# Performance work log

Hardware: AMD Instinct MI355X
Metric: run time of the kernel (lower is better)

## Reference

```python
import jax, jax.numpy as jnp
import numpy as np

N = 200000   # non-empty octree nodes
K = 27       # 3x3x3 neighborhood taps
C = 64       # channels (in == out, stride 1)
EPS = 1e-5


def octree_conv(x, neigh, W):
    # x: [N, Cin], neigh: [N, K] indices into rows of x, W: [K, Cin, Cout]
    g = x[neigh]                      # gather -> [N, K, Cin] (irregular access)
    return jnp.einsum('nkc,kcd->nd', g, W)


def batch_norm(x, gamma, beta):
    # training-mode BatchNorm1d over the node dimension
    mean = jnp.mean(x, axis=0)
    var = jnp.var(x, axis=0)
    return (x - mean) * jax.lax.rsqrt(var + EPS) * gamma + beta


def setup_inputs() -> dict:
    key = jax.random.key(0)
    ks = jax.random.split(key, 4)
    x = jax.random.normal(ks[0], (N, C), dtype=jnp.float32)
    neigh = jax.random.randint(ks[1], (N, K), 0, N, dtype=jnp.int64)
    scale = 1.0 / np.sqrt(K * C)
    W1 = jax.random.normal(ks[2], (K, C, C), dtype=jnp.float32) * scale
    W2 = jax.random.normal(ks[3], (K, C, C), dtype=jnp.float32) * scale
    return {
        'x': x, 'neigh': neigh, 'depth': 5,
        'W1': W1, 'gamma1': jnp.ones((C,), jnp.float32), 'beta1': jnp.zeros((C,), jnp.float32),
        'W2': W2, 'gamma2': jnp.ones((C,), jnp.float32), 'beta2': jnp.zeros((C,), jnp.float32),
    }


def reference(x, neigh, depth, W1, gamma1, beta1, W2, gamma2, beta2):
    residual = x
    out = octree_conv(x, neigh, W1)
    out = jax.nn.relu(batch_norm(out, gamma1, beta1))
    out = octree_conv(out, neigh, W2)   # stride == 1 -> same depth, same neighborhood
    out = batch_norm(out, gamma2, beta2)
    out = jax.nn.relu(out + residual)   # downsample is None for stride 1
    return (out, depth)
```

## Files before the change

### kernel.cpp

```cpp
#include <hip/hip_runtime.h>

typedef __attribute__((ext_vector_type(8))) short bf16x8;
typedef __attribute__((ext_vector_type(4))) float f32x4;

static __device__ __forceinline__ unsigned short f2bf(float f) {
    unsigned int u = __builtin_bit_cast(unsigned int, f);
    u += 0x7fffu + ((u >> 16) & 1u);
    return (unsigned short)(u >> 16);
}
static __device__ __forceinline__ float bf2f(unsigned short h) {
    unsigned int u = ((unsigned int)h) << 16;
    return __builtin_bit_cast(float, u);
}


__global__ void cvt_x_kernel(const float* __restrict__ x, unsigned short* __restrict__ xb, int total8) {
    int i = blockIdx.x * blockDim.x + threadIdx.x;
    if (i >= total8) return;
    const float4* p = reinterpret_cast<const float4*>(x) + (size_t)i * 2;
    float4 a = p[0], b = p[1];
    bf16x8 o;
    o[0] = (short)f2bf(a.x); o[1] = (short)f2bf(a.y); o[2] = (short)f2bf(a.z); o[3] = (short)f2bf(a.w);
    o[4] = (short)f2bf(b.x); o[5] = (short)f2bf(b.y); o[6] = (short)f2bf(b.z); o[7] = (short)f2bf(b.w);
    reinterpret_cast<bf16x8*>(xb)[i] = o;
}

__global__ void cvt_w_kernel(const float* __restrict__ w1, const float* __restrict__ w2,
                             unsigned short* __restrict__ wt1, unsigned short* __restrict__ wt2) {
    int i = blockIdx.x * blockDim.x + threadIdx.x;
    if (i >= 2 * 27 * 4096) return;
    const float* w = (i < 27 * 4096) ? w1 : w2;
    unsigned short* wt = (i < 27 * 4096) ? wt1 : wt2;
    int j = (i < 27 * 4096) ? i : i - 27 * 4096;
    int k = j >> 12;
    int cout = (j >> 6) & 63;
    int cin = j & 63;
    wt[j] = f2bf(w[((size_t)(k * 64 + cin)) * 64 + cout]);
}

__global__ __launch_bounds__(256, 6) void conv_mfma(
    const unsigned short* __restrict__ xb,
    const int* __restrict__ nh,
    const unsigned short* __restrict__ wt,
    unsigned short* __restrict__ y,
    float* __restrict__ pS,
    float* __restrict__ pQ,
    int n)
{
    __shared__ unsigned short Atile[2][4096];
    __shared__ int lidx[27 * 64];

    const int tid  = threadIdx.x;
    const int wid  = tid >> 6;
    const int lane = tid & 63;
    const int lr   = lane & 15;
    const int lg   = lane >> 4;
    const int base = blockIdx.x * 64;

    for (int j = tid; j < 27 * 64; j += 256) {
        int row = j / 27;
        int kk  = j - row * 27;
        int gr  = base + row; if (gr >= n) gr = n - 1;
        lidx[j] = nh[(size_t)gr * 27 + kk];
    }
    __syncthreads();

    const int srow = tid >> 3;
    const int xoff = ((tid & 7) ^ (srow & 7)) * 8;
    const int so0  = srow * 27;
    const int so1  = (srow + 32) * 27;

    f32x4 acc[4];
    #pragma unroll
    for (int t = 0; t < 4; ++t) acc[t] = (f32x4){0.f, 0.f, 0.f, 0.f};

    const unsigned short* wB = wt + (wid * 16 + lr) * 64 + lg * 8;

#define ISSUE_TILE(kk, b) do {                                                        \
        const int i0_ = lidx[so0 + (kk)];                                             \
        const int i1_ = lidx[so1 + (kk)];                                             \
        __builtin_amdgcn_global_load_lds(                                             \
            (const __attribute__((address_space(1))) unsigned int*)(xb + (size_t)i0_ * 64 + xoff), \
            (__attribute__((address_space(3))) unsigned int*)(&Atile[b][wid * 512]), 16, 0, 0);    \
        __builtin_amdgcn_global_load_lds(                                             \
            (const __attribute__((address_space(1))) unsigned int*)(xb + (size_t)i1_ * 64 + xoff), \
            (__attribute__((address_space(3))) unsigned int*)(&Atile[b][2048 + wid * 512]), 16, 0, 0); \
    } while (0)

    auto compute = [&](const unsigned short* At, bf16x8 B0, bf16x8 B1) {
        #pragma unroll
        for (int t = 0; t < 4; ++t) {
            const int row = t * 16 + lr;
            const int sw  = (row & 7) * 8;
            bf16x8 A0 = *reinterpret_cast<const bf16x8*>(&At[row * 64 + ((lg * 8) ^ sw)]);
            bf16x8 A1 = *reinterpret_cast<const bf16x8*>(&At[row * 64 + (((4 + lg) * 8) ^ sw)]);
            acc[t] = __builtin_amdgcn_mfma_f32_16x16x32_bf16(A0, B0, acc[t], 0, 0, 0);
            acc[t] = __builtin_amdgcn_mfma_f32_16x16x32_bf16(A1, B1, acc[t], 0, 0, 0);
        }
    };

    bf16x8 Ba0 = *reinterpret_cast<const bf16x8*>(wB);
    bf16x8 Ba1 = *reinterpret_cast<const bf16x8*>(wB + 32);
    ISSUE_TILE(0, 0);

    for (int k = 0; k < 26; k += 2) {
        bf16x8 Bb0 = *reinterpret_cast<const bf16x8*>(wB + (k + 1) * 4096);
        bf16x8 Bb1 = *reinterpret_cast<const bf16x8*>(wB + (k + 1) * 4096 + 32);
        ISSUE_TILE(k + 1, 1);
        asm volatile("s_waitcnt vmcnt(4)" ::: "memory");
        __builtin_amdgcn_s_barrier();
        __builtin_amdgcn_sched_barrier(0);
        compute(&Atile[0][0], Ba0, Ba1);
        asm volatile("s_waitcnt lgkmcnt(0)" ::: "memory");
        __builtin_amdgcn_sched_barrier(0);
        __builtin_amdgcn_s_barrier();

        Ba0 = *reinterpret_cast<const bf16x8*>(wB + (k + 2) * 4096);
        Ba1 = *reinterpret_cast<const bf16x8*>(wB + (k + 2) * 4096 + 32);
        ISSUE_TILE(k + 2, 0);
        asm volatile("s_waitcnt vmcnt(4)" ::: "memory");
        __builtin_amdgcn_s_barrier();
        __builtin_amdgcn_sched_barrier(0);
        compute(&Atile[1][0], Bb0, Bb1);
        asm volatile("s_waitcnt lgkmcnt(0)" ::: "memory");
        __builtin_amdgcn_sched_barrier(0);
        __builtin_amdgcn_s_barrier();
    }
    asm volatile("s_waitcnt vmcnt(0)" ::: "memory");
    __builtin_amdgcn_s_barrier();
    __builtin_amdgcn_sched_barrier(0);
    compute(&Atile[0][0], Ba0, Ba1);
#undef ISSUE_TILE

    float s1 = 0.f, s2 = 0.f;
    #pragma unroll
    for (int t = 0; t < 4; ++t) {
        #pragma unroll
        for (int rg = 0; rg < 4; ++rg) {
            const int row = base + t * 16 + lg * 4 + rg;
            const float v = acc[t][rg];
            if (row < n) {
                s1 += v;
                s2 += v * v;
                y[(size_t)row * 64 + wid * 16 + lr] = f2bf(v);
            }
        }
    }
    s1 += __shfl_xor(s1, 16); s1 += __shfl_xor(s1, 32);
    s2 += __shfl_xor(s2, 16); s2 += __shfl_xor(s2, 32);
    if (lane < 16) {
        const int ch = wid * 16 + lane;
        pS[(size_t)ch * gridDim.x + blockIdx.x] = s1;
        pQ[(size_t)ch * gridDim.x + blockIdx.x] = s2;
    }
}

__global__ __launch_bounds__(256) void bn_stats_kernel(
        const float* __restrict__ pS, const float* __restrict__ pQ,
        const float* __restrict__ gamma, const float* __restrict__ beta,
        float* __restrict__ bnp, int nb, float invN) {
    const int c = blockIdx.x;
    const int tid = threadIdx.x;
    float S = 0.f, Q = 0.f;
    for (int b = tid; b < nb; b += 256) {
        S += pS[(size_t)c * nb + b];
        Q += pQ[(size_t)c * nb + b];
    }
    #pragma unroll
    for (int o = 1; o < 64; o <<= 1) {
        S += __shfl_xor(S, o);
        Q += __shfl_xor(Q, o);
    }
    __shared__ float sh[8];
    if ((tid & 63) == 0) { sh[(tid >> 6) * 2] = S; sh[(tid >> 6) * 2 + 1] = Q; }
    __syncthreads();
    if (tid == 0) {
        S = sh[0] + sh[2] + sh[4] + sh[6];
        Q = sh[1] + sh[3] + sh[5] + sh[7];
        const float mean = S * invN;
        const float var  = Q * invN - mean * mean;
        const float sc   = gamma[c] * rsqrtf(var + 1e-5f);
        bnp[c]      = sc;
        bnp[64 + c] = beta[c] - mean * sc;
    }
}

__global__ void bn_relu_kernel(const unsigned short* __restrict__ y, const float* __restrict__ bnp,
                               unsigned short* __restrict__ yn, int total8) {
    int i = blockIdx.x * blockDim.x + threadIdx.x;
    if (i >= total8) return;
    bf16x8 v = reinterpret_cast<const bf16x8*>(y)[i];
    int c0 = (i * 8) & 63;
    bf16x8 o;
    #pragma unroll
    for (int j = 0; j < 8; ++j) {
        float f = bf2f((unsigned short)v[j]) * bnp[c0 + j] + bnp[64 + c0 + j];
        f = fmaxf(f, 0.f);
        o[j] = (short)f2bf(f);
    }
    reinterpret_cast<bf16x8*>(yn)[i] = o;
}

__global__ void final_kernel(const unsigned short* __restrict__ y2, const float* __restrict__ x,
                             const float* __restrict__ bnp, const int* __restrict__ depth,
                             float* __restrict__ out, int total8, int n) {
    int i = blockIdx.x * blockDim.x + threadIdx.x;
    if (i == 0) out[(size_t)n * 64] = (float)depth[0];
    if (i >= total8) return;
    bf16x8 v = reinterpret_cast<const bf16x8*>(y2)[i];
    const float4* xp = reinterpret_cast<const float4*>(x) + (size_t)i * 2;
    float4 xa = xp[0], xbv = xp[1];
    int c0 = (i * 8) & 63;
    float r[8];
    #pragma unroll
    for (int j = 0; j < 8; ++j)
        r[j] = bf2f((unsigned short)v[j]) * bnp[c0 + j] + bnp[64 + c0 + j];
    r[0] += xa.x;  r[1] += xa.y;  r[2] += xa.z;  r[3] += xa.w;
    r[4] += xbv.x; r[5] += xbv.y; r[6] += xbv.z; r[7] += xbv.w;
    float4* op = reinterpret_cast<float4*>(out) + (size_t)i * 2;
    float4 o0 = {fmaxf(r[0], 0.f), fmaxf(r[1], 0.f), fmaxf(r[2], 0.f), fmaxf(r[3], 0.f)};
    float4 o1 = {fmaxf(r[4], 0.f), fmaxf(r[5], 0.f), fmaxf(r[6], 0.f), fmaxf(r[7], 0.f)};
    op[0] = o0;
    op[1] = o1;
}

extern "C" void kernel_launch(void* const* d_in, const int* in_sizes, int n_in,
                              void* d_out, int out_size, void* d_ws, size_t ws_size,
                              hipStream_t stream) {
    const float* x     = (const float*)d_in[0];
    const int*   neigh = (const int*)d_in[1];
    const int*   depth = (const int*)d_in[2];
    const float* W1    = (const float*)d_in[3];
    const float* g1    = (const float*)d_in[4];
    const float* b1    = (const float*)d_in[5];
    const float* W2    = (const float*)d_in[6];
    const float* g2    = (const float*)d_in[7];
    const float* b2    = (const float*)d_in[8];
    float* out = (float*)d_out;

    const int n      = in_sizes[0] / 64;
    const int total8 = in_sizes[0] / 8;
    const int nb     = (n + 63) / 64;

    char* ws = (char*)d_ws;
    size_t off = 0;
    auto carve = [&](size_t bytes) -> char* {
        char* p = ws + off;
        off += (bytes + 255) & ~((size_t)255);
        return p;
    };
    unsigned short* bufA = (unsigned short*)carve((size_t)n * 64 * 2);
    unsigned short* bufB = (unsigned short*)carve((size_t)n * 64 * 2);
    unsigned short* w1t  = (unsigned short*)carve(27 * 4096 * 2);
    unsigned short* w2t  = (unsigned short*)carve(27 * 4096 * 2);
    float*          pS   = (float*)carve((size_t)nb * 64 * 4);
    float*          pQ   = (float*)carve((size_t)nb * 64 * 4);
    float*          bnp1 = (float*)carve(128 * 4);
    float*          bnp2 = (float*)carve(128 * 4);

    const int gcvt = (total8 + 255) / 256;
    const int gw   = (2 * 27 * 4096 + 255) / 256;
    const float invN = 1.0f / (float)n;

    cvt_x_kernel<<<gcvt, 256, 0, stream>>>(x, bufA, total8);
    cvt_w_kernel<<<gw, 256, 0, stream>>>(W1, W2, w1t, w2t);

    conv_mfma<<<nb, 256, 0, stream>>>(bufA, neigh, w1t, bufB, pS, pQ, n);
    bn_stats_kernel<<<64, 256, 0, stream>>>(pS, pQ, g1, b1, bnp1, nb, invN);
    bn_relu_kernel<<<gcvt, 256, 0, stream>>>(bufB, bnp1, bufA, total8);

    conv_mfma<<<nb, 256, 0, stream>>>(bufA, neigh, w2t, bufB, pS, pQ, n);
    bn_stats_kernel<<<64, 256, 0, stream>>>(pS, pQ, g2, b2, bnp2, nb, invN);
    final_kernel<<<gcvt, 256, 0, stream>>>(bufB, x, bnp2, depth, out, total8, n);
}
```

Measured before the change: 282.0 us.

## Deepen gather prefetch to four LDS stages and use 2x2 wave tiling

The gathered neighbor rows now go into a four-buffer LDS ring, with three taps prefetched ahead instead of one, and the tap loop is fully unrolled with explicit vmcnt waits. Each wave now computes a 32x32 output sub-tile instead of a 64x16 one, which halves its A-fragment LDS reads and keeps four weight fragments per tap in registers. Per-channel BN partial sums are combined across waves through LDS before they are written out. The aim is to hide irregular gather latency better. The cost is more LDS and registers per block, with the launch-bounds occupancy target lowered from 6 to 4.

```diff
diff --git a/kernel.cpp b/kernel.cpp
--- a/kernel.cpp
+++ b/kernel.cpp
@@ -38,7 +38,7 @@
     wt[j] = f2bf(w[((size_t)(k * 64 + cin)) * 64 + cout]);
 }
 
-__global__ __launch_bounds__(256, 6) void conv_mfma(
+__global__ __launch_bounds__(256, 4) void conv_mfma(
     const unsigned short* __restrict__ xb,
     const int* __restrict__ nh,
     const unsigned short* __restrict__ wt,
@@ -47,7 +47,7 @@
     float* __restrict__ pQ,
     int n)
 {
-    __shared__ unsigned short Atile[2][4096];
+    __shared__ unsigned short Atile[4][4096];
     __shared__ int lidx[27 * 64];
 
     const int tid  = threadIdx.x;
@@ -56,6 +56,8 @@
     const int lr   = lane & 15;
     const int lg   = lane >> 4;
     const int base = blockIdx.x * 64;
+    const int rw   = (wid & 1) * 32;
+    const int cw   = (wid >> 1) * 32;
 
     for (int j = tid; j < 27 * 64; j += 256) {
         int row = j / 27;
@@ -70,88 +72,103 @@
     const int so0  = srow * 27;
     const int so1  = (srow + 32) * 27;
 
-    f32x4 acc[4];
-    #pragma unroll
-    for (int t = 0; t < 4; ++t) acc[t] = (f32x4){0.f, 0.f, 0.f, 0.f};
-
-    const unsigned short* wB = wt + (wid * 16 + lr) * 64 + lg * 8;
-
-#define ISSUE_TILE(kk, b) do {                                                        \
+    f32x4 acc[2][2];
+    acc[0][0] = (f32x4){0.f,0.f,0.f,0.f}; acc[0][1] = (f32x4){0.f,0.f,0.f,0.f};
+    acc[1][0] = (f32x4){0.f,0.f,0.f,0.f}; acc[1][1] = (f32x4){0.f,0.f,0.f,0.f};
+
+    const unsigned short* wB = wt + (size_t)(cw + lr) * 64 + lg * 8;
+    bf16x8 Breg[4][4];
+
+#define ISSUE(kk) do {                                                                \
         const int i0_ = lidx[so0 + (kk)];                                             \
         const int i1_ = lidx[so1 + (kk)];                                             \
+        Breg[(kk)&3][0] = *reinterpret_cast<const bf16x8*>(wB + (kk)*4096);           \
+        Breg[(kk)&3][1] = *reinterpret_cast<const bf16x8*>(wB + (kk)*4096 + 32);      \
+        Breg[(kk)&3][2] = *reinterpret_cast<const bf16x8*>(wB + (kk)*4096 + 1024);    \
+        Breg[(kk)&3][3] = *reinterpret_cast<const bf16x8*>(wB + (kk)*4096 + 1056);    \
         __builtin_amdgcn_global_load_lds(                                             \
             (const __attribute__((address_space(1))) unsigned int*)(xb + (size_t)i0_ * 64 + xoff), \
-            (__attribute__((address_space(3))) unsigned int*)(&Atile[b][wid * 512]), 16, 0, 0);    \
+            (__attribute__((address_space(3))) unsigned int*)(&Atile[(kk)&3][wid * 512]), 16, 0, 0);    \
         __builtin_amdgcn_global_load_lds(                                             \
             (const __attribute__((address_space(1))) unsigned int*)(xb + (size_t)i1_ * 64 + xoff), \
-            (__attribute__((address_space(3))) unsigned int*)(&Atile[b][2048 + wid * 512]), 16, 0, 0); \
+            (__attribute__((address_space(3))) unsigned int*)(&Atile[(kk)&3][2048 + wid * 512]), 16, 0, 0); \
     } while (0)
 
-    auto compute = [&](const unsigned short* At, bf16x8 B0, bf16x8 B1) {
-        #pragma unroll
-        for (int t = 0; t < 4; ++t) {
-            const int row = t * 16 + lr;
-            const int sw  = (row & 7) * 8;
-            bf16x8 A0 = *reinterpret_cast<const bf16x8*>(&At[row * 64 + ((lg * 8) ^ sw)]);
-            bf16x8 A1 = *reinterpret_cast<const bf16x8*>(&At[row * 64 + (((4 + lg) * 8) ^ sw)]);
-            acc[t] = __builtin_amdgcn_mfma_f32_16x16x32_bf16(A0, B0, acc[t], 0, 0, 0);
-            acc[t] = __builtin_amdgcn_mfma_f32_16x16x32_bf16(A1, B1, acc[t], 0, 0, 0);
-        }
-    };
-
-    bf16x8 Ba0 = *reinterpret_cast<const bf16x8*>(wB);
-    bf16x8 Ba1 = *reinterpret_cast<const bf16x8*>(wB + 32);
-    ISSUE_TILE(0, 0);
-
-    for (int k = 0; k < 26; k += 2) {
-        bf16x8 Bb0 = *reinterpret_cast<const bf16x8*>(wB + (k + 1) * 4096);
-        bf16x8 Bb1 = *reinterpret_cast<const bf16x8*>(wB + (k + 1) * 4096 + 32);
-        ISSUE_TILE(k + 1, 1);
-        asm volatile("s_waitcnt vmcnt(4)" ::: "memory");
-        __builtin_amdgcn_s_barrier();
-        __builtin_amdgcn_sched_barrier(0);
-        compute(&Atile[0][0], Ba0, Ba1);
-        asm volatile("s_waitcnt lgkmcnt(0)" ::: "memory");
-        __builtin_amdgcn_sched_barrier(0);
-        __builtin_amdgcn_s_barrier();
-
-        Ba0 = *reinterpret_cast<const bf16x8*>(wB + (k + 2) * 4096);
-        Ba1 = *reinterpret_cast<const bf16x8*>(wB + (k + 2) * 4096 + 32);
-        ISSUE_TILE(k + 2, 0);
-        asm volatile("s_waitcnt vmcnt(4)" ::: "memory");
-        __builtin_amdgcn_s_barrier();
-        __builtin_amdgcn_sched_barrier(0);
-        compute(&Atile[1][0], Bb0, Bb1);
-        asm volatile("s_waitcnt lgkmcnt(0)" ::: "memory");
-        __builtin_amdgcn_sched_barrier(0);
-        __builtin_amdgcn_s_barrier();
-    }
-    asm volatile("s_waitcnt vmcnt(0)" ::: "memory");
-    __builtin_amdgcn_s_barrier();
-    __builtin_amdgcn_sched_barrier(0);
-    compute(&Atile[0][0], Ba0, Ba1);
-#undef ISSUE_TILE
-
-    float s1 = 0.f, s2 = 0.f;
-    #pragma unroll
-    for (int t = 0; t < 4; ++t) {
+#define COMPUTE_BODY(kk) do {                                                         \
+        const unsigned short* At = &Atile[(kk)&3][0];                                 \
+        _Pragma("unroll")                                                             \
+        for (int rf = 0; rf < 2; ++rf) {                                              \
+            const int row_ = rw + rf * 16 + lr;                                       \
+            const int sw_  = (row_ & 7) * 8;                                          \
+            bf16x8 A0 = *reinterpret_cast<const bf16x8*>(&At[row_ * 64 + ((lg * 8) ^ sw_)]);        \
+            bf16x8 A1 = *reinterpret_cast<const bf16x8*>(&At[row_ * 64 + (((4 + lg) * 8) ^ sw_)]);  \
+            acc[rf][0] = __builtin_amdgcn_mfma_f32_16x16x32_bf16(A0, Breg[(kk)&3][0], acc[rf][0], 0, 0, 0); \
+            acc[rf][0] = __builtin_amdgcn_mfma_f32_16x16x32_bf16(A1, Breg[(kk)&3][1], acc[rf][0], 0, 0, 0); \
+            acc[rf][1] = __builtin_amdgcn_mfma_f32_16x16x32_bf16(A0, Breg[(kk)&3][2], acc[rf][1], 0, 0, 0); \
+            acc[rf][1] = __builtin_amdgcn_mfma_f32_16x16x32_bf16(A1, Breg[(kk)&3][3], acc[rf][1], 0, 0, 0); \
+        }                                                                             \
+    } while (0)
+
+#define PHASE(kk, VMSTR) do {                                                         \
+        asm volatile("s_waitcnt " VMSTR ::: "memory");                                \
+        __builtin_amdgcn_s_barrier();                                                 \
+        __builtin_amdgcn_sched_barrier(0);                                            \
+        COMPUTE_BODY(kk);                                                             \
+        asm volatile("s_waitcnt lgkmcnt(0)" ::: "memory");                            \
+        __builtin_amdgcn_sched_barrier(0);                                            \
+        __builtin_amdgcn_s_barrier();                                                 \
+    } while (0)
+
+    ISSUE(0); ISSUE(1); ISSUE(2);
+
+    #pragma unroll
+    for (int k = 0; k < 24; ++k) {
+        ISSUE(k + 3);
+        PHASE(k, "vmcnt(18)");
+    }
+    PHASE(24, "vmcnt(12)");
+    PHASE(25, "vmcnt(6)");
+    PHASE(26, "vmcnt(0)");
+#undef ISSUE
+#undef COMPUTE_BODY
+#undef PHASE
+
+    float s1[2] = {0.f, 0.f}, s2[2] = {0.f, 0.f};
+    #pragma unroll
+    for (int rf = 0; rf < 2; ++rf) {
         #pragma unroll
         for (int rg = 0; rg < 4; ++rg) {
-            const int row = base + t * 16 + lg * 4 + rg;
-            const float v = acc[t][rg];
+            const int row = base + rw + rf * 16 + lg * 4 + rg;
             if (row < n) {
-                s1 += v;
-                s2 += v * v;
-                y[(size_t)row * 64 + wid * 16 + lr] = f2bf(v);
+                #pragma unroll
+                for (int cf = 0; cf < 2; ++cf) {
+                    const float v = acc[rf][cf][rg];
+                    s1[cf] += v;
+                    s2[cf] += v * v;
+                    y[(size_t)row * 64 + cw + cf * 16 + lr] = f2bf(v);
+                }
             }
         }
     }
-    s1 += __shfl_xor(s1, 16); s1 += __shfl_xor(s1, 32);
-    s2 += __shfl_xor(s2, 16); s2 += __shfl_xor(s2, 32);
+    #pragma unroll
+    for (int cf = 0; cf < 2; ++cf) {
+        s1[cf] += __shfl_xor(s1[cf], 16); s1[cf] += __shfl_xor(s1[cf], 32);
+        s2[cf] += __shfl_xor(s2[cf], 16); s2[cf] += __shfl_xor(s2[cf], 32);
+    }
+    float* fs = (float*)&Atile[0][0];
     if (lane < 16) {
-        const int ch = wid * 16 + lane;
-        pS[(size_t)ch * gridDim.x + blockIdx.x] = s1;
-        pQ[(size_t)ch * gridDim.x + blockIdx.x] = s2;
+        fs[wid * 32 + lr]            = s1[0];
+        fs[wid * 32 + 16 + lr]       = s1[1];
+        fs[128 + wid * 32 + lr]      = s2[0];
+        fs[128 + wid * 32 + 16 + lr] = s2[1];
+    }
+    __syncthreads();
+    if (tid < 64) {
+        const int hi = tid >> 5, cl = tid & 31;
+        const float S = fs[hi * 64 + cl] + fs[hi * 64 + 32 + cl];
+        const float Q = fs[128 + hi * 64 + cl] + fs[128 + hi * 64 + 32 + cl];
+        pS[(size_t)tid * gridDim.x + blockIdx.x] = S;
+        pQ[(size_t)tid * gridDim.x + blockIdx.x] = Q;
     }
 }
 
```

New measurement: 428.2 us. 51.9% more time.

## Triple-buffer gathered A tiles to deepen load prefetch in conv kernel

Applied to the files above, without the earlier changes.

Moves the gather-conv main loop from double to triple buffering. The LDS A-tile gets a third 4 KB slot and two tap tiles are kept in flight while a third is computed, with vmcnt waits adjusted to match. Weight loads move into the issue macro, and launch bounds drop from 6 to 5 blocks per CU to make room for the extra LDS and registers. The aim is to hide more irregular gather latency, at the cost of lower occupancy and more outstanding memory operations per wave.

```diff
diff --git a/kernel.cpp b/kernel.cpp
--- a/kernel.cpp
+++ b/kernel.cpp
@@ -38,7 +38,7 @@
     wt[j] = f2bf(w[((size_t)(k * 64 + cin)) * 64 + cout]);
 }
 
-__global__ __launch_bounds__(256, 6) void conv_mfma(
+__global__ __launch_bounds__(256, 5) void conv_mfma(
     const unsigned short* __restrict__ xb,
     const int* __restrict__ nh,
     const unsigned short* __restrict__ wt,
@@ -47,7 +47,7 @@
     float* __restrict__ pQ,
     int n)
 {
-    __shared__ unsigned short Atile[2][4096];
+    __shared__ unsigned short Atile[3][4096];
     __shared__ int lidx[27 * 64];
 
     const int tid  = threadIdx.x;
@@ -75,62 +75,58 @@
     for (int t = 0; t < 4; ++t) acc[t] = (f32x4){0.f, 0.f, 0.f, 0.f};
 
     const unsigned short* wB = wt + (wid * 16 + lr) * 64 + lg * 8;
-
-#define ISSUE_TILE(kk, b) do {                                                        \
+    bf16x8 Ba0, Ba1, Bb0, Bb1, Bc0, Bc1;
+
+#define ISSUE(kk, BUF, B0, B1) do {                                                   \
         const int i0_ = lidx[so0 + (kk)];                                             \
         const int i1_ = lidx[so1 + (kk)];                                             \
+        B0 = *reinterpret_cast<const bf16x8*>(wB + (size_t)(kk) * 4096);              \
+        B1 = *reinterpret_cast<const bf16x8*>(wB + (size_t)(kk) * 4096 + 32);         \
         __builtin_amdgcn_global_load_lds(                                             \
             (const __attribute__((address_space(1))) unsigned int*)(xb + (size_t)i0_ * 64 + xoff), \
-            (__attribute__((address_space(3))) unsigned int*)(&Atile[b][wid * 512]), 16, 0, 0);    \
+            (__attribute__((address_space(3))) unsigned int*)(&Atile[BUF][wid * 512]), 16, 0, 0);    \
         __builtin_amdgcn_global_load_lds(                                             \
             (const __attribute__((address_space(1))) unsigned int*)(xb + (size_t)i1_ * 64 + xoff), \
-            (__attribute__((address_space(3))) unsigned int*)(&Atile[b][2048 + wid * 512]), 16, 0, 0); \
+            (__attribute__((address_space(3))) unsigned int*)(&Atile[BUF][2048 + wid * 512]), 16, 0, 0); \
     } while (0)
 
-    auto compute = [&](const unsigned short* At, bf16x8 B0, bf16x8 B1) {
-        #pragma unroll
-        for (int t = 0; t < 4; ++t) {
-            const int row = t * 16 + lr;
-            const int sw  = (row & 7) * 8;
-            bf16x8 A0 = *reinterpret_cast<const bf16x8*>(&At[row * 64 + ((lg * 8) ^ sw)]);
-            bf16x8 A1 = *reinterpret_cast<const bf16x8*>(&At[row * 64 + (((4 + lg) * 8) ^ sw)]);
-            acc[t] = __builtin_amdgcn_mfma_f32_16x16x32_bf16(A0, B0, acc[t], 0, 0, 0);
-            acc[t] = __builtin_amdgcn_mfma_f32_16x16x32_bf16(A1, B1, acc[t], 0, 0, 0);
-        }
-    };
-
-    bf16x8 Ba0 = *reinterpret_cast<const bf16x8*>(wB);
-    bf16x8 Ba1 = *reinterpret_cast<const bf16x8*>(wB + 32);
-    ISSUE_TILE(0, 0);
-
-    for (int k = 0; k < 26; k += 2) {
-        bf16x8 Bb0 = *reinterpret_cast<const bf16x8*>(wB + (k + 1) * 4096);
-        bf16x8 Bb1 = *reinterpret_cast<const bf16x8*>(wB + (k + 1) * 4096 + 32);
-        ISSUE_TILE(k + 1, 1);
-        asm volatile("s_waitcnt vmcnt(4)" ::: "memory");
-        __builtin_amdgcn_s_barrier();
-        __builtin_amdgcn_sched_barrier(0);
-        compute(&Atile[0][0], Ba0, Ba1);
-        asm volatile("s_waitcnt lgkmcnt(0)" ::: "memory");
-        __builtin_amdgcn_sched_barrier(0);
-        __builtin_amdgcn_s_barrier();
-
-        Ba0 = *reinterpret_cast<const bf16x8*>(wB + (k + 2) * 4096);
-        Ba1 = *reinterpret_cast<const bf16x8*>(wB + (k + 2) * 4096 + 32);
-        ISSUE_TILE(k + 2, 0);
-        asm volatile("s_waitcnt vmcnt(4)" ::: "memory");
-        __builtin_amdgcn_s_barrier();
-        __builtin_amdgcn_sched_barrier(0);
-        compute(&Atile[1][0], Bb0, Bb1);
-        asm volatile("s_waitcnt lgkmcnt(0)" ::: "memory");
-        __builtin_amdgcn_sched_barrier(0);
-        __builtin_amdgcn_s_barrier();
-    }
-    asm volatile("s_waitcnt vmcnt(0)" ::: "memory");
-    __builtin_amdgcn_s_barrier();
-    __builtin_amdgcn_sched_barrier(0);
-    compute(&Atile[0][0], Ba0, Ba1);
-#undef ISSUE_TILE
+#define PHASE(BUF, B0, B1, VMSTR) do {                                                \
+        asm volatile("s_waitcnt " VMSTR ::: "memory");                                \
+        __builtin_amdgcn_s_barrier();                                                 \
+        __builtin_amdgcn_sched_barrier(0);                                            \
+        const unsigned short* At = &Atile[BUF][0];                                    \
+        _Pragma("unroll")                                                             \
+        for (int t = 0; t < 4; ++t) {                                                 \
+            const int row_ = t * 16 + lr;                                             \
+            const int sw_  = (row_ & 7) * 8;                                          \
+            bf16x8 A0 = *reinterpret_cast<const bf16x8*>(&At[row_ * 64 + ((lg * 8) ^ sw_)]);        \
+            bf16x8 A1 = *reinterpret_cast<const bf16x8*>(&At[row_ * 64 + (((4 + lg) * 8) ^ sw_)]);  \
+            acc[t] = __builtin_amdgcn_mfma_f32_16x16x32_bf16(A0, B0, acc[t], 0, 0, 0); \
+            acc[t] = __builtin_amdgcn_mfma_f32_16x16x32_bf16(A1, B1, acc[t], 0, 0, 0); \
+        }                                                                             \
+        asm volatile("s_waitcnt lgkmcnt(0)" ::: "memory");                            \
+        __builtin_amdgcn_sched_barrier(0);                                            \
+        __builtin_amdgcn_s_barrier();                                                 \
+    } while (0)
+
+    ISSUE(0, 0, Ba0, Ba1);
+    ISSUE(1, 1, Bb0, Bb1);
+
+    #pragma unroll 1
+    for (int k = 0; k < 24; k += 3) {
+        ISSUE(k + 2, 2, Bc0, Bc1);
+        PHASE(0, Ba0, Ba1, "vmcnt(8)");
+        ISSUE(k + 3, 0, Ba0, Ba1);
+        PHASE(1, Bb0, Bb1, "vmcnt(8)");
+        ISSUE(k + 4, 1, Bb0, Bb1);
+        PHASE(2, Bc0, Bc1, "vmcnt(8)");
+    }
+    ISSUE(26, 2, Bc0, Bc1);
+    PHASE(0, Ba0, Ba1, "vmcnt(8)");
+    PHASE(1, Bb0, Bb1, "vmcnt(4)");
+    PHASE(2, Bc0, Bc1, "vmcnt(0)");
+#undef ISSUE
+#undef PHASE
 
     float s1 = 0.f, s2 = 0.f;
     #pragma unroll
```

After: 282.5 us. No clear change (+0.2%).
